# Kernel optimization log

Hardware: AMD Instinct MI355X
Metric: run time of the kernel (lower is better)

Reference implementation:

```python
import jax, jax.numpy as jnp
import numpy as np

GRID_SIZE = 5
SPLINE_ORDER = 3
GRID_RANGE = (-1.0, 1.0)


def _make_grid():
    # knots: arange(-k, G+k+1)*h + lo, shared across in_features (uniform grid)
    h = (GRID_RANGE[1] - GRID_RANGE[0]) / GRID_SIZE
    return (jnp.arange(-SPLINE_ORDER, GRID_SIZE + SPLINE_ORDER + 1, dtype=jnp.float32) * h
            + GRID_RANGE[0])  # (G + 2k + 1,) = (12,)


def _b_splines(x2d, grid):
    # x2d: (T, C); grid: (12,) broadcast over features
    x = x2d[..., None]  # (T, C, 1)
    g = grid[None, None, :]  # (1, 1, 12)
    bases = ((x >= g[..., :-1]) & (x < g[..., 1:])).astype(x2d.dtype)
    for k in range(1, SPLINE_ORDER + 1):
        left = (x - g[..., : -(k + 1)]) / (g[..., k:-1] - g[..., : -(k + 1)])
        right = (g[..., k + 1:] - x) / (g[..., k + 1:] - g[..., 1:-k])
        bases = left * bases[..., :-1] + right * bases[..., 1:]
    return bases  # (T, C, G + k) = (T, C, 8)


def setup_inputs() -> dict:
    key = jax.random.key(0)
    k1, k2, k3, k4 = jax.random.split(key, 4)
    B, N, C, O = 4, 4096, 768, 768
    n_coef = GRID_SIZE + SPLINE_ORDER  # 8
    x = jax.random.normal(k1, (B, N, C), dtype=jnp.float32) * 0.5
    base_weight = jax.random.normal(k2, (O, C), dtype=jnp.float32) * (1.0 / np.sqrt(C))
    spline_weight = jax.random.normal(k3, (O, C, n_coef), dtype=jnp.float32) * 0.1
    spline_scaler = jax.random.normal(k4, (O, C), dtype=jnp.float32) * (1.0 / np.sqrt(C))
    return {"x": x, "base_weight": base_weight, "spline_weight": spline_weight,
            "spline_scaler": spline_scaler}


def reference(x, base_weight, spline_weight, spline_scaler):
    B, N, C = x.shape
    x2d = x.reshape(B * N, C)
    grid = _make_grid()
    # base path: SiLU activation + linear
    base_out = jnp.einsum('tc,oc->to', jax.nn.silu(x2d), base_weight)
    # spline path: B-spline bases + scaled linear combination
    bases = _b_splines(x2d, grid)  # (T, C, 8)
    w = spline_weight * spline_scaler[..., None]  # (O, C, 8)
    spline_out = jnp.einsum('tcg,ocg->to', bases, w)
    out = (base_out + spline_out).reshape(B, N, -1)
    return out  # dropout with p=0.0 is identity
```

## Files before the change

kernel.cpp:

```cpp
#include <hip/hip_runtime.h>

typedef __attribute__((ext_vector_type(8)))  short  short8;
typedef __attribute__((ext_vector_type(16))) float  f32x16;
typedef __attribute__((ext_vector_type(4)))  float  flt4;
typedef __attribute__((ext_vector_type(4)))  unsigned int u32x4;

#define T_DIM 16384
#define C_DIM 768
#define O_DIM 768

#define GPC    10
#define CK2    16
#define CHUNKS 48
#define KSTEPS 10
#define NSG    480
#define K2     7680
#define LDA2   168
#define BM     64
#define BN     384
#define LDSBUF 21504
#define WT2_BYTES  ((size_t)O_DIM * K2 * 2)

__device__ __forceinline__ unsigned short f2bf(float f) {
  unsigned u = __float_as_uint(f);
  return (unsigned short)((u + 0x7FFFu + ((u >> 16) & 1u)) >> 16);
}

__device__ __forceinline__ unsigned cvtpk(float lo, float hi) {
  unsigned r;
  asm("v_cvt_pk_bf16_f32 %0, %1, %2" : "=v"(r) : "v"(lo), "v"(hi));
  return r;
}

__global__ void kan_prep2(const float* __restrict__ bw, const float* __restrict__ sw,
                          const float* __restrict__ sc, unsigned short* __restrict__ wt) {
  int id = blockIdx.x * 256 + threadIdx.x;
  if (id >= O_DIM * C_DIM) return;
  int o = id / C_DIM;
  int c = id - o * C_DIM;
  float b = bw[id];
  float s = sc[id];
  const float* sp = sw + (size_t)id * 8;
  int kb = (c >> 4) * 160 + (c & 15) * GPC;
  wt[(size_t)(kb >> 4) * 12288 + o * 16 + (kb & 15)] = f2bf(b);
  {
    int k = kb + 1;
    wt[(size_t)(k >> 4) * 12288 + o * 16 + (k & 15)] = 0;
  }
#pragma unroll
  for (int g = 0; g < 8; ++g) {
    int k = kb + 2 + g;
    wt[(size_t)(k >> 4) * 12288 + o * 16 + (k & 15)] = f2bf(sp[g] * s);
  }
}

__global__ __launch_bounds__(256, 2) void kan_gemm5(
    const float* __restrict__ x, const unsigned short* __restrict__ wt,
    float* __restrict__ out) {
  __shared__ short Alds[2 * BM * LDA2];

  const int tid  = threadIdx.x;
  const int lane = tid & 63;
  const int wn   = tid >> 6;
  const int l31  = lane & 31;
  const int lq   = lane >> 5;

  const int d  = blockIdx.x;
  const int yt = d & 1;
  const int xt = d >> 1;
  const int tBase = xt * BM;
  const int oBase = yt * BN + wn * 96;

  f32x16 acc[2][3];
#pragma unroll
  for (int a = 0; a < 2; ++a)
#pragma unroll
    for (int b = 0; b < 3; ++b)
#pragma unroll
      for (int r = 0; r < 16; ++r) acc[a][b][r] = 0.0f;

  const int sRow = tid >> 2;
  const int sSb  = tid & 3;
  const float* xrow = x + (size_t)(tBase + sRow) * C_DIM + sSb * 4;

  char* ldsB = (char*)Alds;
  const int wbase = sRow * 336 + sSb * 80;
  int rbyte[2];
#pragma unroll
  for (int mf = 0; mf < 2; ++mf)
    rbyte[mf] = (mf * 32 + l31) * 336 + lq * 16;

  flt4 xa = *(const flt4*)(xrow);
  unsigned wds[20];

  auto stage_j = [&](int j) {
    float xx  = xa[j];
    float ex  = __expf(-xx);
    float sig = __builtin_amdgcn_rcpf(1.0f + ex);
    wds[5 * j] = cvtpk(xx * sig, 0.0f);
    float u  = fmaf(xx, 2.5f, 5.5f);
    float fl = floorf(u);
    int   jj = (int)fl;
    float f  = u - fl;
    float f2 = f * f, f3 = f2 * f;
    float W0 = f3 * (1.0f / 6.0f);
    float om = 1.0f - f;
    float W3 = om * om * om * (1.0f / 6.0f);
    float W2 = 0.5f * f3 - f2 + (2.0f / 3.0f);
    float W1 = 1.0f - W0 - W2 - W3;
    unsigned V0 = cvtpk(W3, W2);
    unsigned V1 = cvtpk(W1, W0);
    unsigned A0 = V0 << 16;
    unsigned A1 = (V1 << 16) | (V0 >> 16);
    unsigned A2 = V1 >> 16;
    int  k = jj - 3;
    int  q = k >> 1;
    bool r = (k & 1) != 0;
    unsigned U0 = r ? A0 : V0;
    unsigned U1 = r ? A1 : V1;
    unsigned U2 = r ? A2 : 0u;
#pragma unroll
    for (int p = 0; p < 4; ++p)
      wds[5 * j + 1 + p] =
          (q == p) ? U0 : ((q == p - 1) ? U1 : ((q == p - 2) ? U2 : 0u));
  };

#define WRITE_ONE(I, WOFF)                                              \
  {                                                                     \
    u32x4 t;                                                            \
    t.x = wds[4 * (I)];     t.y = wds[4 * (I) + 1];                     \
    t.z = wds[4 * (I) + 2]; t.w = wds[4 * (I) + 3];                     \
    *(u32x4*)(ldsB + (WOFF) + wbase + (I) * 16) = t;                    \
  }

#pragma unroll
  for (int j = 0; j < 4; ++j) stage_j(j);
  WRITE_ONE(0, 0) WRITE_ONE(1, 0) WRITE_ONE(2, 0) WRITE_ONE(3, 0) WRITE_ONE(4, 0)
  xa = *(const flt4*)(xrow + CK2);

  const size_t lofs = (size_t)(oBase + l31) * 16 + lq * 8;
  short8 bb0[3], bb1[3];
  {
    const unsigned short* w0 = wt + lofs;
    bb0[0] = *(const short8*)(w0);
    bb0[1] = *(const short8*)(w0 + 512);
    bb0[2] = *(const short8*)(w0 + 1024);
    const unsigned short* w1 = wt + 12288 + lofs;
    bb1[0] = *(const short8*)(w1);
    bb1[1] = *(const short8*)(w1 + 512);
    bb1[2] = *(const short8*)(w1 + 1024);
  }
  __syncthreads();

#define LDSA(MF, KS) (*(const short8*)(ldsB + roff + rbyte[MF] + (KS) * 32))
#define MFMA(A, B, C) __builtin_amdgcn_mfma_f32_32x32x16_bf16((A), (B), (C), 0, 0, 0)

  short8 aa0[2], aa1[2];

#define KSTEP(KS, BB, AAC, AAN, DOREAD, SJ, WR, DOX, GUARD)              \
  {                                                                      \
    if (DOREAD) {                                                        \
      AAN[0] = LDSA(0, (KS) + 1);                                        \
      AAN[1] = LDSA(1, (KS) + 1);                                        \
    }                                                                    \
    __builtin_amdgcn_s_setprio(1);                                       \
    acc[0][0] = MFMA(AAC[0], BB[0], acc[0][0]);                          \
    acc[0][1] = MFMA(AAC[0], BB[1], acc[0][1]);                          \
    acc[0][2] = MFMA(AAC[0], BB[2], acc[0][2]);                          \
    acc[1][0] = MFMA(AAC[1], BB[0], acc[1][0]);                          \
    acc[1][1] = MFMA(AAC[1], BB[1], acc[1][1]);                          \
    acc[1][2] = MFMA(AAC[1], BB[2], acc[1][2]);                          \
    __builtin_amdgcn_s_setprio(0);                                       \
    if (!(GUARD) || (chBase + (KS) + 2 < NSG)) {                         \
      const unsigned short* wp =                                         \
          wt + (size_t)(chBase + (KS) + 2) * 12288 + lofs;               \
      BB[0] = *(const short8*)(wp);                                      \
      BB[1] = *(const short8*)(wp + 512);                                \
      BB[2] = *(const short8*)(wp + 1024);                               \
    }                                                                    \
    if ((WR) >= 0) WRITE_ONE((WR) < 0 ? 0 : (WR), woff)                  \
    if ((SJ) >= 0) stage_j(SJ);                                          \
    if (DOX) xa = *(const flt4*)(xrow + (ch + 2) * CK2);                 \
  }

  for (int ch = 0; ch < CHUNKS - 1; ++ch) {
    const int chBase = ch * KSTEPS;
    const int roff   = (ch & 1) * LDSBUF;
    const int woff   = roff ^ LDSBUF;
    const bool dox   = (ch + 2 < CHUNKS);
    aa0[0] = LDSA(0, 0);
    aa0[1] = LDSA(1, 0);
    KSTEP(0, bb0, aa0, aa1, 1,  0, -1, false, 0)
    KSTEP(1, bb1, aa1, aa0, 1,  1, -1, false, 0)
    KSTEP(2, bb0, aa0, aa1, 1,  2, -1, false, 0)
    KSTEP(3, bb1, aa1, aa0, 1,  3, -1, false, 0)
    KSTEP(4, bb0, aa0, aa1, 1, -1,  0, dox,   0)
    KSTEP(5, bb1, aa1, aa0, 1, -1,  1, false, 0)
    KSTEP(6, bb0, aa0, aa1, 1, -1,  2, false, 0)
    KSTEP(7, bb1, aa1, aa0, 1, -1,  3, false, 0)
    KSTEP(8, bb0, aa0, aa1, 1, -1,  4, false, 0)
    KSTEP(9, bb1, aa1, aa0, 0, -1, -1, false, 0)
    __syncthreads();
  }
  {
    const int ch     = CHUNKS - 1;
    (void)ch;
    const int chBase = (CHUNKS - 1) * KSTEPS;
    const int roff   = ((CHUNKS - 1) & 1) * LDSBUF;
    const int woff   = roff ^ LDSBUF;
    (void)woff;
    aa0[0] = LDSA(0, 0);
    aa0[1] = LDSA(1, 0);
    KSTEP(0, bb0, aa0, aa1, 1, -1, -1, false, 1)
    KSTEP(1, bb1, aa1, aa0, 1, -1, -1, false, 1)
    KSTEP(2, bb0, aa0, aa1, 1, -1, -1, false, 1)
    KSTEP(3, bb1, aa1, aa0, 1, -1, -1, false, 1)
    KSTEP(4, bb0, aa0, aa1, 1, -1, -1, false, 1)
    KSTEP(5, bb1, aa1, aa0, 1, -1, -1, false, 1)
    KSTEP(6, bb0, aa0, aa1, 1, -1, -1, false, 1)
    KSTEP(7, bb1, aa1, aa0, 1, -1, -1, false, 1)
    KSTEP(8, bb0, aa0, aa1, 1, -1, -1, false, 1)
    KSTEP(9, bb1, aa1, aa0, 0, -1, -1, false, 1)
  }

#undef KSTEP
#undef LDSA
#undef MFMA
#undef WRITE_ONE

#pragma unroll
  for (int mf = 0; mf < 2; ++mf) {
    int tRow0 = tBase + mf * 32 + 4 * lq;
#pragma unroll
    for (int nf = 0; nf < 3; ++nf) {
      int oCol = oBase + nf * 32 + l31;
#pragma unroll
      for (int r = 0; r < 16; ++r) {
        int rowf = (r & 3) + 8 * (r >> 2);
        out[(size_t)(tRow0 + rowf) * O_DIM + oCol] = acc[mf][nf][r];
      }
    }
  }
}

__global__ __launch_bounds__(256, 2) void kan_gemm_fb(
    const float* __restrict__ x, const float* __restrict__ bw,
    const float* __restrict__ sw, const float* __restrict__ sc,
    float* __restrict__ out) {
  __shared__ short Alds[128 * 152];
  const int tid  = threadIdx.x;
  const int lane = tid & 63;
  const int wave = tid >> 6;
  const int wm   = wave >> 1;
  const int wn   = wave & 1;
  const int l31  = lane & 31;
  const int lq   = lane >> 5;
  const int tBase = blockIdx.x * 128;
  const int oBase = blockIdx.y * 192 + wn * 96;
  f32x16 acc[2][3];
#pragma unroll
  for (int a = 0; a < 2; ++a)
#pragma unroll
    for (int b = 0; b < 3; ++b)
#pragma unroll
      for (int r = 0; r < 16; ++r) acc[a][b][r] = 0.0f;
  const int sRow = tid >> 1;
  const int sSb  = tid & 1;
  const float* xrow = x + (size_t)(tBase + sRow) * C_DIM + sSb * 8;
  for (int ch = 0; ch < 48; ++ch) {
    __syncthreads();
    const float* xp = xrow + ch * 16;
    flt4 xv0 = *(const flt4*)(xp);
    flt4 xv1 = *(const flt4*)(xp + 4);
    short8 plane[9];
#pragma unroll
    for (int j = 0; j < 8; ++j) {
      float xx  = (j < 4) ? xv0[j] : xv1[j - 4];
      float sig = 1.0f / (1.0f + __expf(-xx));
      plane[0][j] = f2bf(xx * sig);
      float u  = fmaf(xx, 2.5f, 5.5f);
      float fl = floorf(u);
      int   jj = (int)fl;
      float f  = u - fl;
      float f2 = f * f, f3 = f2 * f;
      float W0 = f3 * (1.0f / 6.0f);
      float om = 1.0f - f;
      float W3 = om * om * om * (1.0f / 6.0f);
      float W2 = 0.5f * f3 - f2 + (2.0f / 3.0f);
      float W1 = 1.0f - W0 - W2 - W3;
#pragma unroll
      for (int s = 0; s < 8; ++s) {
        int   dd  = jj - s;
        float v01 = (dd & 1) ? W1 : W0;
        float v23 = (dd & 1) ? W3 : W2;
        float v   = (dd & 2) ? v23 : v01;
        v = ((unsigned)dd < 4u) ? v : 0.0f;
        plane[1 + s][j] = f2bf(v);
      }
    }
    {
      short* arow = &Alds[sRow * 152 + sSb * 72];
#pragma unroll
      for (int g = 0; g < 9; ++g) *(short8*)(arow + g * 8) = plane[g];
    }
    __syncthreads();
    for (int ks = 0; ks < 9; ++ks) {
      const int sGlob = ch * 9 + ks;
      short8 bfr[3];
      const int h    = sGlob * 2 + lq;
      const int cblk = (h * 7282) >> 16;
      const int g    = h - cblk * 9;
      const int cb   = cblk * 8;
#pragma unroll
      for (int nf = 0; nf < 3; ++nf) {
        int col = oBase + nf * 32 + l31;
        const float* rowb = ((g == 0) ? bw : sc) + (size_t)col * C_DIM + cb;
        flt4 s0 = *(const flt4*)rowb;
        flt4 s1 = *(const flt4*)(rowb + 4);
        short8 v;
        if (g == 0) {
#pragma unroll
          for (int j = 0; j < 8; ++j) v[j] = f2bf((j < 4) ? s0[j] : s1[j - 4]);
        } else {
          const float* sp = sw + ((size_t)col * C_DIM + cb) * 8 + (g - 1);
#pragma unroll
          for (int j = 0; j < 8; ++j) {
            float scv = (j < 4) ? s0[j] : s1[j - 4];
            v[j] = f2bf(sp[j * 8] * scv);
          }
        }
        bfr[nf] = v;
      }
      short8 afr[2];
#pragma unroll
      for (int mf = 0; mf < 2; ++mf)
        afr[mf] = *(const short8*)&Alds[(wm * 64 + mf * 32 + l31) * 152 + ks * 16 + lq * 8];
#pragma unroll
      for (int mf = 0; mf < 2; ++mf)
#pragma unroll
        for (int nf = 0; nf < 3; ++nf)
          acc[mf][nf] = __builtin_amdgcn_mfma_f32_32x32x16_bf16(
              afr[mf], bfr[nf], acc[mf][nf], 0, 0, 0);
    }
  }
#pragma unroll
  for (int mf = 0; mf < 2; ++mf) {
    int tRow0 = tBase + wm * 64 + mf * 32 + 4 * lq;
#pragma unroll
    for (int nf = 0; nf < 3; ++nf) {
      int oCol = oBase + nf * 32 + l31;
#pragma unroll
      for (int r = 0; r < 16; ++r) {
        int rowf = (r & 3) + 8 * (r >> 2);
        out[(size_t)(tRow0 + rowf) * O_DIM + oCol] = acc[mf][nf][r];
      }
    }
  }
}

extern "C" void kernel_launch(void* const* d_in, const int* in_sizes, int n_in,
                              void* d_out, int out_size, void* d_ws, size_t ws_size,
                              hipStream_t stream) {
  const float* x  = (const float*)d_in[0];
  const float* bw = (const float*)d_in[1];
  const float* sw = (const float*)d_in[2];
  const float* sc = (const float*)d_in[3];
  float* out = (float*)d_out;

  const bool use_ws = (d_ws != nullptr) && (ws_size >= WT2_BYTES);
  if (use_ws) {
    unsigned short* wt = (unsigned short*)d_ws;
    kan_prep2<<<(O_DIM * C_DIM + 255) / 256, 256, 0, stream>>>(bw, sw, sc, wt);
    kan_gemm5<<<dim3((T_DIM / BM) * (O_DIM / BN)), 256, 0, stream>>>(x, wt, out);
  } else {
    kan_gemm_fb<<<dim3(T_DIM / 128, O_DIM / 192), 256, 0, stream>>>(x, bw, sw, sc, out);
  }
}
```

Before: 206.7 us.

## Pack K dimension densely: drop padding slot, 9 k-steps per chunk with triple B buffering

The fused K layout drops the per-channel zero padding. The old layout gave each of the 16 channels 10 slots (silu, zero, 8 bases). The new one groups 16 silu values followed by 16×8 basis weights, so K shrinks from 7680 to 6912 and each chunk needs 9 MFMA k-steps instead of 10. Weight prep and the LDS staging writes are rearranged to match, and B-fragment prefetching now rotates three register buffers with a lookahead of 3. The aim is to cut MFMA work and weight bandwidth by about 10%, at the cost of more VGPR pressure from the extra buffer and a changed LDS write pattern.

```diff
diff --git a/kernel.cpp b/kernel.cpp
--- a/kernel.cpp
+++ b/kernel.cpp
@@ -4,22 +4,22 @@
 typedef __attribute__((ext_vector_type(16))) float  f32x16;
 typedef __attribute__((ext_vector_type(4)))  float  flt4;
 typedef __attribute__((ext_vector_type(4)))  unsigned int u32x4;
+typedef __attribute__((ext_vector_type(2)))  unsigned int u32x2;
 
 #define T_DIM 16384
 #define C_DIM 768
 #define O_DIM 768
 
-#define GPC    10
 #define CK2    16
 #define CHUNKS 48
-#define KSTEPS 10
-#define NSG    480
-#define K2     7680
-#define LDA2   168
+#define KSTEPS 9
+#define NSG    432
+#define K3     6912
+#define LDA3   152
 #define BM     64
 #define BN     384
-#define LDSBUF 21504
-#define WT2_BYTES  ((size_t)O_DIM * K2 * 2)
+#define LDSBUF 19456
+#define WT3_BYTES  ((size_t)NSG * 12288 * 2)
 
 __device__ __forceinline__ unsigned short f2bf(float f) {
   unsigned u = __float_as_uint(f);
@@ -32,7 +32,7 @@
   return r;
 }
 
-__global__ void kan_prep2(const float* __restrict__ bw, const float* __restrict__ sw,
+__global__ void kan_prep3(const float* __restrict__ bw, const float* __restrict__ sw,
                           const float* __restrict__ sc, unsigned short* __restrict__ wt) {
   int id = blockIdx.x * 256 + threadIdx.x;
   if (id >= O_DIM * C_DIM) return;
@@ -41,23 +41,21 @@
   float b = bw[id];
   float s = sc[id];
   const float* sp = sw + (size_t)id * 8;
-  int kb = (c >> 4) * 160 + (c & 15) * GPC;
-  wt[(size_t)(kb >> 4) * 12288 + o * 16 + (kb & 15)] = f2bf(b);
   {
-    int k = kb + 1;
-    wt[(size_t)(k >> 4) * 12288 + o * 16 + (k & 15)] = 0;
+    int k = (c >> 4) * 144 + (c & 15);
+    wt[(size_t)(k >> 4) * 12288 + o * 16 + (k & 15)] = f2bf(b);
   }
 #pragma unroll
   for (int g = 0; g < 8; ++g) {
-    int k = kb + 2 + g;
+    int k = (c >> 4) * 144 + 16 + (c & 15) * 8 + g;
     wt[(size_t)(k >> 4) * 12288 + o * 16 + (k & 15)] = f2bf(sp[g] * s);
   }
 }
 
-__global__ __launch_bounds__(256, 2) void kan_gemm5(
+__global__ __launch_bounds__(256, 2) void kan_gemm6(
     const float* __restrict__ x, const unsigned short* __restrict__ wt,
     float* __restrict__ out) {
-  __shared__ short Alds[2 * BM * LDA2];
+  __shared__ short Alds[2 * BM * LDA3];
 
   const int tid  = threadIdx.x;
   const int lane = tid & 63;
@@ -84,20 +82,21 @@
   const float* xrow = x + (size_t)(tBase + sRow) * C_DIM + sSb * 4;
 
   char* ldsB = (char*)Alds;
-  const int wbase = sRow * 336 + sSb * 80;
+  const int wbase = sRow * 304;
   int rbyte[2];
 #pragma unroll
   for (int mf = 0; mf < 2; ++mf)
-    rbyte[mf] = (mf * 32 + l31) * 336 + lq * 16;
+    rbyte[mf] = (mf * 32 + l31) * 304 + lq * 16;
 
   flt4 xa = *(const flt4*)(xrow);
-  unsigned wds[20];
+  float    su[4];
+  unsigned sww[16];
 
   auto stage_j = [&](int j) {
     float xx  = xa[j];
     float ex  = __expf(-xx);
     float sig = __builtin_amdgcn_rcpf(1.0f + ex);
-    wds[5 * j] = cvtpk(xx * sig, 0.0f);
+    su[j] = xx * sig;
     float u  = fmaf(xx, 2.5f, 5.5f);
     float fl = floorf(u);
     int   jj = (int)fl;
@@ -121,16 +120,22 @@
     unsigned U2 = r ? A2 : 0u;
 #pragma unroll
     for (int p = 0; p < 4; ++p)
-      wds[5 * j + 1 + p] =
+      sww[4 * j + p] =
           (q == p) ? U0 : ((q == p - 1) ? U1 : ((q == p - 2) ? U2 : 0u));
   };
 
-#define WRITE_ONE(I, WOFF)                                              \
+#define WRITE_ONE(WR, WOFF)                                             \
   {                                                                     \
-    u32x4 t;                                                            \
-    t.x = wds[4 * (I)];     t.y = wds[4 * (I) + 1];                     \
-    t.z = wds[4 * (I) + 2]; t.w = wds[4 * (I) + 3];                     \
-    *(u32x4*)(ldsB + (WOFF) + wbase + (I) * 16) = t;                    \
+    if ((WR) == 0) {                                                    \
+      u32x2 t;                                                          \
+      t.x = cvtpk(su[0], su[1]); t.y = cvtpk(su[2], su[3]);             \
+      *(u32x2*)(ldsB + (WOFF) + wbase + sSb * 8) = t;                   \
+    } else {                                                            \
+      u32x4 t;                                                          \
+      t.x = sww[4 * ((WR) - 1)];     t.y = sww[4 * ((WR) - 1) + 1];     \
+      t.z = sww[4 * ((WR) - 1) + 2]; t.w = sww[4 * ((WR) - 1) + 3];     \
+      *(u32x4*)(ldsB + (WOFF) + wbase + 32 + sSb * 64 + ((WR) - 1) * 16) = t; \
+    }                                                                   \
   }
 
 #pragma unroll
@@ -139,7 +144,7 @@
   xa = *(const flt4*)(xrow + CK2);
 
   const size_t lofs = (size_t)(oBase + l31) * 16 + lq * 8;
-  short8 bb0[3], bb1[3];
+  short8 bb0[3], bb1[3], bb2[3];
   {
     const unsigned short* w0 = wt + lofs;
     bb0[0] = *(const short8*)(w0);
@@ -149,6 +154,10 @@
     bb1[0] = *(const short8*)(w1);
     bb1[1] = *(const short8*)(w1 + 512);
     bb1[2] = *(const short8*)(w1 + 1024);
+    const unsigned short* w2 = wt + 24576 + lofs;
+    bb2[0] = *(const short8*)(w2);
+    bb2[1] = *(const short8*)(w2 + 512);
+    bb2[2] = *(const short8*)(w2 + 1024);
   }
   __syncthreads();
 
@@ -171,14 +180,14 @@
     acc[1][1] = MFMA(AAC[1], BB[1], acc[1][1]);                          \
     acc[1][2] = MFMA(AAC[1], BB[2], acc[1][2]);                          \
     __builtin_amdgcn_s_setprio(0);                                       \
-    if (!(GUARD) || (chBase + (KS) + 2 < NSG)) {                         \
+    if (!(GUARD) || (chBase + (KS) + 3 < NSG)) {                         \
       const unsigned short* wp =                                         \
-          wt + (size_t)(chBase + (KS) + 2) * 12288 + lofs;               \
+          wt + (size_t)(chBase + (KS) + 3) * 12288 + lofs;               \
       BB[0] = *(const short8*)(wp);                                      \
       BB[1] = *(const short8*)(wp + 512);                                \
       BB[2] = *(const short8*)(wp + 1024);                               \
     }                                                                    \
-    if ((WR) >= 0) WRITE_ONE((WR) < 0 ? 0 : (WR), woff)                  \
+    if ((WR) >= 0) WRITE_ONE(WR, woff)                                   \
     if ((SJ) >= 0) stage_j(SJ);                                          \
     if (DOX) xa = *(const flt4*)(xrow + (ch + 2) * CK2);                 \
   }
@@ -192,14 +201,13 @@
     aa0[1] = LDSA(1, 0);
     KSTEP(0, bb0, aa0, aa1, 1,  0, -1, false, 0)
     KSTEP(1, bb1, aa1, aa0, 1,  1, -1, false, 0)
-    KSTEP(2, bb0, aa0, aa1, 1,  2, -1, false, 0)
-    KSTEP(3, bb1, aa1, aa0, 1,  3, -1, false, 0)
-    KSTEP(4, bb0, aa0, aa1, 1, -1,  0, dox,   0)
-    KSTEP(5, bb1, aa1, aa0, 1, -1,  1, false, 0)
+    KSTEP(2, bb2, aa0, aa1, 1,  2, -1, false, 0)
+    KSTEP(3, bb0, aa1, aa0, 1,  3, -1, false, 0)
+    KSTEP(4, bb1, aa0, aa1, 1, -1,  0, dox,   0)
+    KSTEP(5, bb2, aa1, aa0, 1, -1,  1, false, 0)
     KSTEP(6, bb0, aa0, aa1, 1, -1,  2, false, 0)
     KSTEP(7, bb1, aa1, aa0, 1, -1,  3, false, 0)
-    KSTEP(8, bb0, aa0, aa1, 1, -1,  4, false, 0)
-    KSTEP(9, bb1, aa1, aa0, 0, -1, -1, false, 0)
+    KSTEP(8, bb2, aa0, aa1, 0, -1,  4, false, 0)
     __syncthreads();
   }
   {
@@ -207,20 +215,19 @@
     (void)ch;
     const int chBase = (CHUNKS - 1) * KSTEPS;
     const int roff   = ((CHUNKS - 1) & 1) * LDSBUF;
-    const int woff   = roff ^ LDSBUF;
+    const int woff   = 0;
     (void)woff;
     aa0[0] = LDSA(0, 0);
     aa0[1] = LDSA(1, 0);
     KSTEP(0, bb0, aa0, aa1, 1, -1, -1, false, 1)
     KSTEP(1, bb1, aa1, aa0, 1, -1, -1, false, 1)
-    KSTEP(2, bb0, aa0, aa1, 1, -1, -1, false, 1)
-    KSTEP(3, bb1, aa1, aa0, 1, -1, -1, false, 1)
-    KSTEP(4, bb0, aa0, aa1, 1, -1, -1, false, 1)
-    KSTEP(5, bb1, aa1, aa0, 1, -1, -1, false, 1)
+    KSTEP(2, bb2, aa0, aa1, 1, -1, -1, false, 1)
+    KSTEP(3, bb0, aa1, aa0, 1, -1, -1, false, 1)
+    KSTEP(4, bb1, aa0, aa1, 1, -1, -1, false, 1)
+    KSTEP(5, bb2, aa1, aa0, 1, -1, -1, false, 1)
     KSTEP(6, bb0, aa0, aa1, 1, -1, -1, false, 1)
     KSTEP(7, bb1, aa1, aa0, 1, -1, -1, false, 1)
-    KSTEP(8, bb0, aa0, aa1, 1, -1, -1, false, 1)
-    KSTEP(9, bb1, aa1, aa0, 0, -1, -1, false, 1)
+    KSTEP(8, bb2, aa0, aa1, 0, -1, -1, false, 1)
   }
 
 #undef KSTEP
@@ -367,11 +374,11 @@
   const float* sc = (const float*)d_in[3];
   float* out = (float*)d_out;
 
-  const bool use_ws = (d_ws != nullptr) && (ws_size >= WT2_BYTES);
+  const bool use_ws = (d_ws != nullptr) && (ws_size >= WT3_BYTES);
   if (use_ws) {
     unsigned short* wt = (unsigned short*)d_ws;
-    kan_prep2<<<(O_DIM * C_DIM + 255) / 256, 256, 0, stream>>>(bw, sw, sc, wt);
-    kan_gemm5<<<dim3((T_DIM / BM) * (O_DIM / BN)), 256, 0, stream>>>(x, wt, out);
+    kan_prep3<<<(O_DIM * C_DIM + 255) / 256, 256, 0, stream>>>(bw, sw, sc, wt);
+    kan_gemm6<<<dim3((T_DIM / BM) * (O_DIM / BN)), 256, 0, stream>>>(x, wt, out);
   } else {
     kan_gemm_fb<<<dim3(T_DIM / 128, O_DIM / 192), 256, 0, stream>>>(x, bw, sw, sc, out);
   }
```

Measured after the change: 179.0 us. -13.4%, faster.
